# Optimization experiments

Hardware: AMD Instinct MI355X
Metric: run time of the kernel (lower is better)

Reference implementation:

```python
import jax, jax.numpy as jnp
import numpy as np

S, B, D, H, E, K, DF = 1024, 16, 512, 8, 16, 2, 2048
HD = D // H
EPS = 1e-5


def _layernorm(x, g, b):
    m = x.mean(-1, keepdims=True)
    v = ((x - m) ** 2).mean(-1, keepdims=True)
    return (x - m) / jnp.sqrt(v + EPS) * g + b


def setup_inputs() -> dict:
    key = jax.random.key(0)
    ks = jax.random.split(key, 10)
    s = 0.02
    return {
        "src": jax.random.normal(ks[0], (S, B, D), jnp.float32),
        "pos": jax.random.normal(ks[1], (S, B, D), jnp.float32),
        "in_proj_w": jax.random.normal(ks[2], (3 * D, D), jnp.float32) * s,
        "in_proj_b": jnp.zeros((3 * D,), jnp.float32),
        "out_w": jax.random.normal(ks[3], (D, D), jnp.float32) * s,
        "out_b": jnp.zeros((D,), jnp.float32),
        "norm1_g": jnp.ones((D,), jnp.float32),
        "norm1_b": jnp.zeros((D,), jnp.float32),
        "gate_w": jax.random.normal(ks[4], (E, D), jnp.float32) * s,
        "gate_b": jnp.zeros((E,), jnp.float32),
        "w1": jax.random.normal(ks[5], (E, DF, D), jnp.float32) * s,
        "b1": jnp.zeros((E, DF), jnp.float32),
        "w2": jax.random.normal(ks[6], (E, D, DF), jnp.float32) * s,
        "b2": jnp.zeros((E, D), jnp.float32),
    }


def reference(src, pos, in_proj_w, in_proj_b, out_w, out_b, norm1_g, norm1_b,
              gate_w, gate_b, w1, b1, w2, b2):
    # ---- self attention (torch nn.MultiheadAttention, seq-first) ----
    qk_in = src + pos                      # q = k = src + pos, v = src
    wq, wk, wv = jnp.split(in_proj_w, 3, axis=0)
    bq, bk, bv = jnp.split(in_proj_b, 3, axis=0)
    q = qk_in @ wq.T + bq                  # [S,B,D]
    k = qk_in @ wk.T + bk
    v = src @ wv.T + bv

    def heads(x):                          # [S,B,D] -> [B,H,S,HD]
        return x.reshape(S, B, H, HD).transpose(1, 2, 0, 3)

    qh, kh, vh = heads(q), heads(k), heads(v)
    scores = jnp.einsum('bhqd,bhkd->bhqk', qh * (1.0 / np.sqrt(HD)), kh)
    attn = jax.nn.softmax(scores, axis=-1)
    o = jnp.einsum('bhqk,bhkd->bhqd', attn, vh)
    o = o.transpose(2, 0, 1, 3).reshape(S, B, D) @ out_w.T + out_b

    x = _layernorm(src + o, norm1_g, norm1_b)  # post-norm residual

    # ---- MoE FFN (FMoE NaiveGate, top-k=2, no capacity drop) ----
    t = x.reshape(S * B, D)                # tokens
    logits = t @ gate_w.T + gate_b         # [T,E]
    topv, topi = jax.lax.top_k(logits, K)  # [T,K]
    gate_score = jax.nn.softmax(topv, axis=-1)
    T = S * B
    comb = jnp.zeros((T, E), t.dtype).at[jnp.arange(T)[:, None], topi].add(gate_score)

    def body(acc, packed):
        W1, B1, W2, B2, c = packed         # per-expert weights + combine col [T]
        h = jax.nn.relu(t @ W1.T + B1)     # [T,DF]
        y = h @ W2.T + B2                  # [T,D]
        return acc + c[:, None] * y, None

    acc, _ = jax.lax.scan(body, jnp.zeros_like(t), (w1, b1, w2, b2, comb.T))
    # pre_lnorm=False branch: output = inp + core_out (internal LN unused)
    return x + acc.reshape(S, B, D)
```

## Files before the change

kernel.cpp:

```cpp
#include <hip/hip_runtime.h>
#include <hip/hip_bf16.h>

typedef float f4 __attribute__((ext_vector_type(4)));
typedef float f32x4 __attribute__((ext_vector_type(4)));
typedef short short8 __attribute__((ext_vector_type(8)));
typedef unsigned short u16x4 __attribute__((ext_vector_type(4)));
typedef unsigned short u16x8 __attribute__((ext_vector_type(8)));
typedef unsigned int u32x4 __attribute__((ext_vector_type(4)));
typedef unsigned int u32x8 __attribute__((ext_vector_type(8)));

#define S_LEN 1024
#define BATCH 16
#define DIM   512
#define NH    8
#define HDIM  64
#define NE    16
#define DFF   2048
#define T_TOK 16384
#define CAP   34816
#define BM    128

__device__ __forceinline__ unsigned short f2bf(float f) {
  union { float f; unsigned u; } v; v.f = f;
  unsigned r = v.u + 0x7fffu + ((v.u >> 16) & 1u);
  return (unsigned short)(r >> 16);
}
__device__ __forceinline__ float bf2f(unsigned short h) {
  union { unsigned u; float f; } v; v.u = ((unsigned)h) << 16;
  return v.f;
}

__device__ __forceinline__ void load_lds16(const void* g, void* l) {
  __builtin_amdgcn_global_load_lds(
      (__attribute__((address_space(1))) void*)(void*)g,
      (__attribute__((address_space(3))) void*)l, 16, 0, 0);
}

__device__ __forceinline__ short8 pack_hi8(const unsigned* val) {
  union { unsigned u[4]; short8 s; } t;
#pragma unroll
  for (int i = 0; i < 4; i++)
    t.u[i] = (val[2 * i] >> 16) | (val[2 * i + 1] & 0xFFFF0000u);
  return t.s;
}
__device__ __forceinline__ short8 pack_lo8(const unsigned* val) {
  union { unsigned u[4]; short8 s; } t;
#pragma unroll
  for (int i = 0; i < 4; i++)
    t.u[i] = (val[2 * i] & 0xFFFFu) | (val[2 * i + 1] << 16);
  return t.s;
}

__global__ __launch_bounds__(256) void k_cvt_bf16(const float* __restrict__ in,
                                                  unsigned short* __restrict__ outb,
                                                  size_t n) {
  size_t i = ((size_t)blockIdx.x * 256 + threadIdx.x) * 4;
  size_t stride = (size_t)gridDim.x * 1024;
  for (; i < n; i += stride) {
    f4 v = *(const f4*)&in[i];
    u16x4 o;
    o[0] = f2bf(v[0]); o[1] = f2bf(v[1]); o[2] = f2bf(v[2]); o[3] = f2bf(v[3]);
    *(u16x4*)&outb[i] = o;
  }
}

__global__ __launch_bounds__(256) void k_split_w(const float* __restrict__ in,
                                                 unsigned short* __restrict__ hi,
                                                 unsigned short* __restrict__ lo,
                                                 size_t n) {
  size_t i = ((size_t)blockIdx.x * 256 + threadIdx.x) * 4;
  size_t stride = (size_t)gridDim.x * 1024;
  for (; i < n; i += stride) {
    f4 v = *(const f4*)&in[i];
    u16x4 h, l;
#pragma unroll
    for (int j = 0; j < 4; j++) {
      unsigned short hh = f2bf(v[j]);
      h[j] = hh;
      l[j] = f2bf(v[j] - bf2f(hh));
    }
    *(u16x4*)&hi[i] = h;
    *(u16x4*)&lo[i] = l;
  }
}

__global__ __launch_bounds__(64) void k_init(int* __restrict__ counts) {
  if (threadIdx.x < NE) counts[threadIdx.x] = 0;
}

__global__ __launch_bounds__(256) void k_zero_pad(const int* __restrict__ counts,
                                                  const int* __restrict__ off_pad,
                                                  unsigned short* __restrict__ Xg) {
  const int e = blockIdx.x;
  const int start = off_pad[e] + counts[e];
  const int end = off_pad[e + 1];
  for (int row = start; row < end; row++)
    *(unsigned int*)&Xg[(size_t)row * DIM + threadIdx.x * 2] = 0u;
}

__global__ __launch_bounds__(256, 2) void k_gemm_split(
    const float* __restrict__ A, const float* __restrict__ A2,
    const unsigned short* __restrict__ Wh, const unsigned short* __restrict__ Wl,
    const float* __restrict__ bias, int epi,
    unsigned* __restrict__ p0, unsigned* __restrict__ p1) {
  __shared__ __align__(16) char smem[33792];
  unsigned short* AhL = (unsigned short*)smem;
  unsigned short* AlL = (unsigned short*)(smem + 8192);
  unsigned short* WhL = (unsigned short*)(smem + 16384);
  unsigned short* WlL = (unsigned short*)(smem + 24576);
  unsigned* bounce = (unsigned*)smem;
  const int tid = threadIdx.x, lane = tid & 63, wid = tid >> 6;
  const int wm = wid >> 1, wn = wid & 1;
  const int m0 = blockIdx.x * 128, n0 = blockIdx.y * 128;
  const int row = tid >> 1, half = tid & 1;
  const int xr = (row >> 1) & 3;
  f32x4 acc[4][4] = {};
  f4 ar[4];
#pragma unroll
  for (int j = 0; j < 4; j++) {
    const size_t aoff = (size_t)(m0 + row) * 512 + half * 16 + j * 4;
    ar[j] = *(const f4*)&A[aoff];
    if (A2) { f4 v2 = *(const f4*)&A2[aoff]; ar[j] += v2; }
  }
  for (int k0 = 0; k0 < 512; k0 += 32) {
    __syncthreads();
    u16x8 hi8[2], lo8[2];
#pragma unroll
    for (int j = 0; j < 16; j++) {
      const float x = ar[j >> 2][j & 3];
      const unsigned short h = f2bf(x);
      hi8[j >> 3][j & 7] = h;
      lo8[j >> 3][j & 7] = f2bf(x - bf2f(h));
    }
    const int c0 = half * 2;
    *(u16x8*)&AhL[row * 32 + (((c0 + 0) ^ xr) << 3)] = hi8[0];
    *(u16x8*)&AhL[row * 32 + (((c0 + 1) ^ xr) << 3)] = hi8[1];
    *(u16x8*)&AlL[row * 32 + (((c0 + 0) ^ xr) << 3)] = lo8[0];
    *(u16x8*)&AlL[row * 32 + (((c0 + 1) ^ xr) << 3)] = lo8[1];
#pragma unroll
    for (int i = 0; i < 2; i++) {
      const int rowW = i * 64 + wid * 16 + (lane >> 2);
      const int clog = (lane & 3) ^ ((rowW >> 1) & 3);
      const size_t woff = (size_t)(n0 + rowW) * 512 + k0 + (clog << 3);
      load_lds16(Wh + woff, &WhL[i * 2048 + wid * 512]);
      load_lds16(Wl + woff, &WlL[i * 2048 + wid * 512]);
    }
    __syncthreads();
    if (k0 + 32 < 512) {
#pragma unroll
      for (int j = 0; j < 4; j++) {
        const size_t aoff = (size_t)(m0 + row) * 512 + k0 + 32 + half * 16 + j * 4;
        ar[j] = *(const f4*)&A[aoff];
        if (A2) { f4 v2 = *(const f4*)&A2[aoff]; ar[j] += v2; }
      }
    }
    const int l15 = lane & 15, lk = lane >> 4;
    const int xa = (l15 >> 1) & 3;
    short8 avh[4], avl[4], bvh[4], bvl[4];
#pragma unroll
    for (int mi = 0; mi < 4; mi++) {
      const int mr = wm * 64 + mi * 16 + l15;
      avh[mi] = *(const short8*)&AhL[mr * 32 + ((lk ^ xa) << 3)];
      avl[mi] = *(const short8*)&AlL[mr * 32 + ((lk ^ xa) << 3)];
    }
#pragma unroll
    for (int ni = 0; ni < 4; ni++) {
      const int nr = wn * 64 + ni * 16 + l15;
      bvh[ni] = *(const short8*)&WhL[nr * 32 + ((lk ^ xa) << 3)];
      bvl[ni] = *(const short8*)&WlL[nr * 32 + ((lk ^ xa) << 3)];
    }
#pragma unroll
    for (int mi = 0; mi < 4; mi++) {
#pragma unroll
      for (int ni = 0; ni < 4; ni++) {
        acc[mi][ni] = __builtin_amdgcn_mfma_f32_16x16x32_bf16(avh[mi], bvh[ni], acc[mi][ni], 0, 0, 0);
        acc[mi][ni] = __builtin_amdgcn_mfma_f32_16x16x32_bf16(avh[mi], bvl[ni], acc[mi][ni], 0, 0, 0);
        acc[mi][ni] = __builtin_amdgcn_mfma_f32_16x16x32_bf16(avl[mi], bvh[ni], acc[mi][ni], 0, 0, 0);
      }
    }
  }
  const int l15 = lane & 15, lq = lane >> 4;
  if (epi == 2) {
    float* of = (float*)p0;
#pragma unroll
    for (int mi = 0; mi < 4; mi++) {
      const int rb = m0 + wm * 64 + mi * 16 + (lq << 2);
#pragma unroll
      for (int ni = 0; ni < 4; ni++) {
        const int n = n0 + wn * 64 + ni * 16 + l15;
        const float bn = bias[n];
#pragma unroll
        for (int r = 0; r < 4; r++)
          of[(size_t)(rb + r) * 512 + n] = acc[mi][ni][r] + bn;
      }
    }
  } else if (epi == 0) {
#pragma unroll
    for (int mi = 0; mi < 4; mi++) {
      const int rb = m0 + wm * 64 + mi * 16 + (lq << 2);
#pragma unroll
      for (int ni = 0; ni < 4; ni++) {
        const int n = n0 + wn * 64 + ni * 16 + l15;
        const float bn = bias[n];
#pragma unroll
        for (int r = 0; r < 4; r++) {
          const int m = rb + r;
          const int bidx = m & 15, ss = m >> 4;
          float v = acc[mi][ni][r] + bn;
          unsigned* pl;
          int nn;
          if (n < 512) { v *= 0.125f; pl = p0; nn = n; }
          else { pl = p1; nn = n - 512; }
          const size_t off = ((size_t)(bidx * NH + (nn >> 6)) * S_LEN + ss) * HDIM + (nn & 63);
          const unsigned short hh = f2bf(v);
          pl[off] = ((unsigned)hh << 16) | (unsigned)f2bf(v - bf2f(hh));
        }
      }
    }
  } else {
    const int s_base = m0 >> 4;
    for (int halfn = 0; halfn < 2; halfn++) {
      __syncthreads();
      if (wn == halfn) {
#pragma unroll
        for (int mi = 0; mi < 4; mi++) {
          const int mlb = wm * 64 + mi * 16 + (lq << 2);
#pragma unroll
          for (int ni = 0; ni < 4; ni++) {
            const int n = n0 + wn * 64 + ni * 16 + l15;
            const float bn = bias[n];
            const int nc = ni * 16 + l15;
#pragma unroll
            for (int r = 0; r < 4; r++) {
              const float v = acc[mi][ni][r] + bn;
              const unsigned short hh = f2bf(v);
              bounce[(mlb + r) * 66 + nc] =
                  ((unsigned)hh << 16) | (unsigned)f2bf(v - bf2f(hh));
            }
          }
        }
      }
      __syncthreads();
#pragma unroll
      for (int i = 0; i < 4; i++) {
        const int idx = tid + 256 * i;
        const int nc = idx & 63, bb = idx >> 6;
        const int ng = n0 + halfn * 64 + nc;
        const int hh_ = ng >> 6, dd = ng & 63;
        u32x8 vals;
#pragma unroll
        for (int s = 0; s < 8; s++) vals[s] = bounce[(s * 16 + bb) * 66 + nc];
        *(u32x8*)&p0[((size_t)(bb * NH + hh_) * HDIM + dd) * S_LEN + s_base] = vals;
      }
    }
  }
}

__global__ __launch_bounds__(256, 4) void k_attn(
    const unsigned* __restrict__ Qp, const unsigned* __restrict__ Kp,
    const unsigned* __restrict__ Vp, float* __restrict__ O) {
  const int q0 = blockIdx.x * 64;
  const int bh = blockIdx.y;
  const int b = bh >> 3, h = bh & 7;
  const size_t base = (size_t)bh * (S_LEN * HDIM);
  __shared__ unsigned short KhL[64][72], KlL[64][72];
  __shared__ unsigned short VhL[64][72], VlL[64][72];
  const int tid = threadIdx.x, lane = tid & 63, w = tid >> 6;
  const int l15 = lane & 15, lq = lane >> 4;
  const int srcA = l15 + 16 * ((2 * lq) & 3);
  const int srcB = l15 + 16 * ((2 * lq + 1) & 3);
  const bool selHi = (lane & 32) != 0;
  short8 qh[2], ql[2];
  {
    const size_t qoff = base + (size_t)(q0 + 16 * w + l15) * HDIM + lq * 8;
    u32x8 qv0 = *(const u32x8*)&Qp[qoff];
    u32x8 qv1 = *(const u32x8*)&Qp[qoff + 32];
    qh[0] = pack_hi8((const unsigned*)&qv0); ql[0] = pack_lo8((const unsigned*)&qv0);
    qh[1] = pack_hi8((const unsigned*)&qv1); ql[1] = pack_lo8((const unsigned*)&qv1);
  }
  const int sr = tid >> 2, sq = (tid & 3) * 16;
  u32x4 kr[4], vr[4];
  {
    const size_t ko = base + (size_t)sr * HDIM + sq;
    const size_t vo = base + (size_t)sr * S_LEN + sq;
#pragma unroll
    for (int i = 0; i < 4; i++) {
      kr[i] = *(const u32x4*)&Kp[ko + 4 * i];
      vr[i] = *(const u32x4*)&Vp[vo + 4 * i];
    }
  }
  float m_ = -1e30f, l_ = 0.f;
  f32x4 acc[4] = {};

  for (int kt = 0; kt < 16; kt++) {
    {
      const unsigned* ku = (const unsigned*)kr;
      const unsigned* vu = (const unsigned*)vr;
      *(short8*)&KhL[sr][sq + 0] = pack_hi8(ku);
      *(short8*)&KhL[sr][sq + 8] = pack_hi8(ku + 8);
      *(short8*)&KlL[sr][sq + 0] = pack_lo8(ku);
      *(short8*)&KlL[sr][sq + 8] = pack_lo8(ku + 8);
      *(short8*)&VhL[sr][sq + 0] = pack_hi8(vu);
      *(short8*)&VhL[sr][sq + 8] = pack_hi8(vu + 8);
      *(short8*)&VlL[sr][sq + 0] = pack_lo8(vu);
      *(short8*)&VlL[sr][sq + 8] = pack_lo8(vu + 8);
    }
    __syncthreads();
    if (kt < 15) {
      const int s0n = (kt + 1) * 64;
      const size_t ko = base + (size_t)(s0n + sr) * HDIM + sq;
      const size_t vo = base + (size_t)sr * S_LEN + s0n + sq;
#pragma unroll
      for (int i = 0; i < 4; i++) {
        kr[i] = *(const u32x4*)&Kp[ko + 4 * i];
        vr[i] = *(const u32x4*)&Vp[vo + 4 * i];
      }
    }
    f32x4 sc[4] = {};
#pragma unroll
    for (int c = 0; c < 2; c++) {
      short8 kfh[4], kfl[4];
#pragma unroll
      for (int n = 0; n < 4; n++) {
        kfh[n] = *(const short8*)&KhL[16 * n + l15][c * 32 + lq * 8];
        kfl[n] = *(const short8*)&KlL[16 * n + l15][c * 32 + lq * 8];
      }
#pragma unroll
      for (int n = 0; n < 4; n++) {
        sc[n] = __builtin_amdgcn_mfma_f32_16x16x32_bf16(kfh[n], qh[c], sc[n], 0, 0, 0);
        sc[n] = __builtin_amdgcn_mfma_f32_16x16x32_bf16(kfl[n], qh[c], sc[n], 0, 0, 0);
        sc[n] = __builtin_amdgcn_mfma_f32_16x16x32_bf16(kfh[n], ql[c], sc[n], 0, 0, 0);
      }
    }
    float tm = fmaxf(fmaxf(fmaxf(sc[0][0], sc[0][1]), fmaxf(sc[0][2], sc[0][3])),
                     fmaxf(fmaxf(sc[1][0], sc[1][1]), fmaxf(sc[1][2], sc[1][3])));
    tm = fmaxf(tm, fmaxf(fmaxf(fmaxf(sc[2][0], sc[2][1]), fmaxf(sc[2][2], sc[2][3])),
                         fmaxf(fmaxf(sc[3][0], sc[3][1]), fmaxf(sc[3][2], sc[3][3]))));
    tm = fmaxf(tm, __shfl_xor(tm, 16));
    tm = fmaxf(tm, __shfl_xor(tm, 32));
    const float mn = fmaxf(m_, tm);
    const float esc = __expf(m_ - mn);
    m_ = mn;
    float rs = 0.f;
    unsigned pk[4][4];
#pragma unroll
    for (int n = 0; n < 4; n++) {
#pragma unroll
      for (int r = 0; r < 4; r++) {
        const float p = __expf(sc[n][r] - mn);
        rs += p;
        const unsigned short hh = f2bf(p);
        pk[n][r] = ((unsigned)hh << 16) | (unsigned)f2bf(p - bf2f(hh));
      }
    }
    rs += __shfl_xor(rs, 16);
    rs += __shfl_xor(rs, 32);
    l_ = l_ * esc + rs;
    float escR[4];
#pragma unroll
    for (int r = 0; r < 4; r++) escR[r] = __shfl(esc, 4 * lq + r);
#pragma unroll
    for (int n = 0; n < 4; n++) {
#pragma unroll
      for (int r = 0; r < 4; r++) acc[n][r] *= escR[r];
    }
#pragma unroll
    for (int c = 0; c < 2; c++) {
      unsigned val[8];
#pragma unroll
      for (int j = 0; j < 8; j++) {
        const int src = (j >> 2) ? srcB : srcA;
        const unsigned sA = (unsigned)__shfl((int)pk[2 * c + 0][j & 3], src);
        const unsigned sB = (unsigned)__shfl((int)pk[2 * c + 1][j & 3], src);
        val[j] = selHi ? sB : sA;
      }
      const short8 ph = pack_hi8(val);
      const short8 plo = pack_lo8(val);
      short8 vfh[4], vfl[4];
#pragma unroll
      for (int n = 0; n < 4; n++) {
        vfh[n] = *(const short8*)&VhL[16 * n + l15][c * 32 + lq * 8];
        vfl[n] = *(const short8*)&VlL[16 * n + l15][c * 32 + lq * 8];
      }
#pragma unroll
      for (int n = 0; n < 4; n++) {
        acc[n] = __builtin_amdgcn_mfma_f32_16x16x32_bf16(ph, vfh[n], acc[n], 0, 0, 0);
        acc[n] = __builtin_amdgcn_mfma_f32_16x16x32_bf16(ph, vfl[n], acc[n], 0, 0, 0);
        acc[n] = __builtin_amdgcn_mfma_f32_16x16x32_bf16(plo, vfh[n], acc[n], 0, 0, 0);
      }
    }
    __syncthreads();
  }
  const float inv = 1.f / l_;
  float invR[4];
#pragma unroll
  for (int r = 0; r < 4; r++) invR[r] = __shfl(inv, 4 * lq + r);
#pragma unroll
  for (int r = 0; r < 4; r++) {
    const int srow = q0 + 16 * w + 4 * lq + r;
    float* orow = &O[((size_t)srow * BATCH + b) * DIM + h * HDIM];
#pragma unroll
    for (int n = 0; n < 4; n++) orow[16 * n + l15] = acc[n][r] * invR[r];
  }
}

__global__ __launch_bounds__(256) void k_ln(const float* __restrict__ src,
                                            const float* __restrict__ proj,
                                            const float* __restrict__ g,
                                            const float* __restrict__ bt,
                                            float* __restrict__ xout) {
  const int wid = threadIdx.x >> 6, lane = threadIdx.x & 63;
  const int tok = blockIdx.x * 4 + wid;
  const size_t base = (size_t)tok * DIM + lane * 8;
  f4 a0 = *(const f4*)&src[base],  a1 = *(const f4*)&src[base + 4];
  f4 p0 = *(const f4*)&proj[base], p1 = *(const f4*)&proj[base + 4];
  float x[8];
  x[0] = a0[0] + p0[0]; x[1] = a0[1] + p0[1]; x[2] = a0[2] + p0[2]; x[3] = a0[3] + p0[3];
  x[4] = a1[0] + p1[0]; x[5] = a1[1] + p1[1]; x[6] = a1[2] + p1[2]; x[7] = a1[3] + p1[3];
  float s = 0.f, sq = 0.f;
#pragma unroll
  for (int j = 0; j < 8; j++) { s += x[j]; sq = fmaf(x[j], x[j], sq); }
#pragma unroll
  for (int d = 1; d < 64; d <<= 1) { s += __shfl_xor(s, d); sq += __shfl_xor(sq, d); }
  const float mean = s * (1.f / 512.f);
  const float var = sq * (1.f / 512.f) - mean * mean;
  const float rstd = 1.f / sqrtf(var + 1e-5f);
  const int ci = lane * 8;
  f4 o0v, o1v;
#pragma unroll
  for (int j = 0; j < 4; j++) o0v[j] = (x[j] - mean) * rstd * g[ci + j] + bt[ci + j];
#pragma unroll
  for (int j = 0; j < 4; j++) o1v[j] = (x[4 + j] - mean) * rstd * g[ci + 4 + j] + bt[ci + 4 + j];
  *(f4*)&xout[base] = o0v;
  *(f4*)&xout[base + 4] = o1v;
}

__global__ __launch_bounds__(256) void k_gate(const float* __restrict__ x,
                                              const float* __restrict__ gw,
                                              const float* __restrict__ gb,
                                              int* __restrict__ topi,
                                              float* __restrict__ topw,
                                              int* __restrict__ counts) {
  __shared__ float xs[16 * 520];
  __shared__ int hist[16];
  const int tid = threadIdx.x;
  const int tl = tid >> 4, e = tid & 15;
  if (tid < 16) hist[tid] = 0;
  const float gbe = gb[e];
  const float* wrow = gw + (size_t)e * DIM;
  for (int tile = 0; tile < 4; tile++) {
    const int t0 = blockIdx.x * 64 + tile * 16;
    __syncthreads();
    {
      const int r = tid >> 4, cbase = (tid & 15) * 32;
#pragma unroll
      for (int j = 0; j < 8; j++) {
        const int c = cbase + j * 4;
        const int ch = c >> 2;
        const int pc = ch ^ ((ch >> 3) & 7);
        *(f4*)&xs[r * 520 + pc * 4] = *(const f4*)&x[(size_t)(t0 + r) * DIM + c];
      }
    }
    __syncthreads();
    float d = gbe;
#pragma unroll 8
    for (int c = 0; c < DIM; c += 4) {
      const int ch = c >> 2;
      const int pc = ch ^ ((ch >> 3) & 7);
      f4 xv = *(const f4*)&xs[tl * 520 + pc * 4];
      f4 wv = *(const f4*)&wrow[c];
      d = fmaf(xv[0], wv[0], d); d = fmaf(xv[1], wv[1], d);
      d = fmaf(xv[2], wv[2], d); d = fmaf(xv[3], wv[3], d);
    }
    float v1 = d, v2 = -1e30f;
    int i1 = e, i2 = 1000;
#pragma unroll
    for (int s = 1; s < 16; s <<= 1) {
      const float ov1 = __shfl_xor(v1, s), ov2 = __shfl_xor(v2, s);
      const int oi1 = __shfl_xor(i1, s), oi2 = __shfl_xor(i2, s);
      if (ov1 > v1 || (ov1 == v1 && oi1 < i1)) {
        float nv2; int ni2;
        if (v1 > ov2 || (v1 == ov2 && i1 < oi2)) { nv2 = v1; ni2 = i1; }
        else { nv2 = ov2; ni2 = oi2; }
        v1 = ov1; i1 = oi1; v2 = nv2; i2 = ni2;
      } else if (ov1 > v2 || (ov1 == v2 && oi1 < i2)) {
        v2 = ov1; i2 = oi1;
      }
    }
    if (e == 0) {
      const int t = t0 + tl;
      const float e1 = __expf(v2 - v1);
      const float inv = 1.f / (1.f + e1);
      topi[2 * t] = i1;  topi[2 * t + 1] = i2;
      topw[2 * t] = inv; topw[2 * t + 1] = e1 * inv;
      atomicAdd(&hist[i1], 1);
      atomicAdd(&hist[i2], 1);
    }
  }
  __syncthreads();
  if (tid < 16 && hist[tid] > 0) atomicAdd(&counts[tid], hist[tid]);
}

__global__ void k_offsets(const int* __restrict__ counts,
                          int* __restrict__ off_pad, int* __restrict__ cursor) {
  if (threadIdx.x == 0) {
    int o = 0;
    off_pad[0] = 0;
    for (int e = 0; e < NE; e++) {
      cursor[e] = 0;
      o += ((counts[e] + BM - 1) / BM) * BM;
      off_pad[e + 1] = o;
    }
  }
}

__global__ __launch_bounds__(256) void k_scatter(const float* __restrict__ x,
                                                 const int* __restrict__ topi,
                                                 const int* __restrict__ off_pad,
                                                 int* __restrict__ cursor,
                                                 int* __restrict__ tokSlot,
                                                 unsigned short* __restrict__ Xg) {
  __shared__ int lcnt[16];
  __shared__ int gbase[16];
  __shared__ int posArr[128];
  const int tid = threadIdx.x;
  const int a0 = blockIdx.x * 128;
  if (tid < 16) lcnt[tid] = 0;
  __syncthreads();
  if (tid < 128) {
    const int a = a0 + tid;
    const int e = topi[a];
    const int lrank = atomicAdd(&lcnt[e], 1);
    posArr[tid] = (e << 24) | lrank;
  }
  __syncthreads();
  if (tid < 16) {
    const int c = lcnt[tid];
    gbase[tid] = (c > 0) ? atomicAdd(&cursor[tid], c) : 0;
  }
  __syncthreads();
  if (tid < 128) {
    const int a = a0 + tid;
    const int pk = posArr[tid];
    const int e = pk >> 24, lrank = pk & 0xffffff;
    const int pos = off_pad[e] + gbase[e] + lrank;
    posArr[tid] = pos;
    tokSlot[a] = pos;
  }
  __syncthreads();
  const int w = tid >> 6, lane = tid & 63;
#pragma unroll 4
  for (int i = 0; i < 32; i++) {
    const int idx = w * 32 + i;
    const int pos = posArr[idx];
    const int tok = (a0 + idx) >> 1;
    const size_t sb = (size_t)tok * DIM + lane * 8;
    f4 v0 = *(const f4*)&x[sb], v1 = *(const f4*)&x[sb + 4];
    u16x8 hh;
    hh[0] = f2bf(v0[0]); hh[1] = f2bf(v0[1]); hh[2] = f2bf(v0[2]); hh[3] = f2bf(v0[3]);
    hh[4] = f2bf(v1[0]); hh[5] = f2bf(v1[1]); hh[6] = f2bf(v1[2]); hh[7] = f2bf(v1[3]);
    *(u16x8*)&Xg[(size_t)pos * DIM + lane * 8] = hh;
  }
}

__global__ __launch_bounds__(256) void k_gemm_bf16(
    const unsigned short* __restrict__ A, int lda,
    const unsigned short* __restrict__ Wb, size_t westride, int ldw, int wrow0,
    const float* __restrict__ bias, int bstride, int brow0,
    int K, int epi,
    unsigned short* __restrict__ Hout, int ldh,
    const int* __restrict__ off_pad) {
  int bx = blockIdx.x;
  const int nwg = gridDim.x;
  if ((nwg & 7) == 0) bx = (bx & 7) * (nwg >> 3) + (bx >> 3);
  const int m0 = bx * BM;
  if (m0 >= off_pad[NE]) return;
  int e = 0;
  while (off_pad[e + 1] <= m0) e++;
  const unsigned short* W = Wb + (size_t)e * westride;
  const int n0 = blockIdx.y * 128;
  __shared__ unsigned short Al[128 * 64];
  __shared__ unsigned short Bl[128 * 64];
  const int tid = threadIdx.x, lane = tid & 63, wid = tid >> 6;
  const int wm = wid >> 1, wn = wid & 1;
  f32x4 acc[4][4] = {};
  const int srow = wid * 32 + (lane >> 3);
  const int scol = (((lane & 7) ^ ((lane >> 3) & 7)) << 3);
  for (int k0 = 0; k0 < K; k0 += 64) {
    const unsigned short* ga = A + (size_t)(m0 + srow) * lda + k0 + scol;
    const unsigned short* gw = W + (size_t)(wrow0 + n0 + srow) * ldw + k0 + scol;
#pragma unroll
    for (int i = 0; i < 4; i++) {
      load_lds16(ga + (size_t)i * 8 * lda, &Al[(wid * 32 + i * 8) * 64]);
      load_lds16(gw + (size_t)i * 8 * ldw, &Bl[(wid * 32 + i * 8) * 64]);
    }
    __syncthreads();
#pragma unroll
    for (int kk = 0; kk < 2; kk++) {
      short8 av[4], bv[4];
      const int ckx = (kk * 4 + (lane >> 4)) ^ (lane & 7);
#pragma unroll
      for (int mi = 0; mi < 4; mi++)
        av[mi] = *(const short8*)&Al[(wm * 64 + mi * 16 + (lane & 15)) * 64 + ckx * 8];
#pragma unroll
      for (int ni = 0; ni < 4; ni++)
        bv[ni] = *(const short8*)&Bl[(wn * 64 + ni * 16 + (lane & 15)) * 64 + ckx * 8];
#pragma unroll
      for (int mi = 0; mi < 4; mi++) {
#pragma unroll
        for (int ni = 0; ni < 4; ni++)
          acc[mi][ni] = __builtin_amdgcn_mfma_f32_16x16x32_bf16(av[mi], bv[ni], acc[mi][ni], 0, 0, 0);
      }
    }
    __syncthreads();
  }
#pragma unroll
  for (int mi = 0; mi < 4; mi++) {
    const int rb = m0 + wm * 64 + mi * 16 + ((lane >> 4) << 2);
#pragma unroll
    for (int ni = 0; ni < 4; ni++) {
      const int n = n0 + wn * 64 + ni * 16 + (lane & 15);
      const float bn = (epi != 2) ? bias[(size_t)e * bstride + brow0 + n] : 0.f;
      if (epi == 0) {
#pragma unroll
        for (int r = 0; r < 4; r++) {
          float v = acc[mi][ni][r] + bn;
          v = fmaxf(v, 0.f);
          Hout[(size_t)(rb + r) * ldh + n] = f2bf(v);
        }
      } else if (epi == 1) {
#pragma unroll
        for (int r = 0; r < 4; r++)
          Hout[(size_t)(rb + r) * ldh + n] = f2bf(acc[mi][ni][r] + bn);
      } else {
#pragma unroll
        for (int r = 0; r < 4; r++) {
          const size_t yo = (size_t)(rb + r) * ldh + n;
          Hout[yo] = f2bf(acc[mi][ni][r] + bf2f(Hout[yo]));
        }
      }
    }
  }
}

__global__ __launch_bounds__(256) void k_combine(const unsigned short* __restrict__ Y,
                                                 const int* __restrict__ tokSlot,
                                                 const float* __restrict__ topw,
                                                 float* __restrict__ out) {
  const int wid = threadIdx.x >> 6, lane = threadIdx.x & 63;
  const int t = blockIdx.x * 4 + wid;
  const int pa = tokSlot[2 * t], pb = tokSlot[2 * t + 1];
  const float wa = topw[2 * t], wb = topw[2 * t + 1];
  const size_t ob = (size_t)t * DIM + lane * 8;
  u16x8 ya = *(const u16x8*)&Y[(size_t)pa * DIM + lane * 8];
  u16x8 yb = *(const u16x8*)&Y[(size_t)pb * DIM + lane * 8];
  f4 o0 = *(const f4*)&out[ob], o1 = *(const f4*)&out[ob + 4];
#pragma unroll
  for (int j = 0; j < 4; j++) o0[j] += wa * bf2f(ya[j]) + wb * bf2f(yb[j]);
#pragma unroll
  for (int j = 0; j < 4; j++) o1[j] += wa * bf2f(ya[4 + j]) + wb * bf2f(yb[4 + j]);
  *(f4*)&out[ob] = o0;
  *(f4*)&out[ob + 4] = o1;
}

extern "C" void kernel_launch(void* const* d_in, const int* in_sizes, int n_in,
                              void* d_out, int out_size, void* d_ws, size_t ws_size,
                              hipStream_t stream) {
  const float* src       = (const float*)d_in[0];
  const float* pos       = (const float*)d_in[1];
  const float* in_proj_w = (const float*)d_in[2];
  const float* in_proj_b = (const float*)d_in[3];
  const float* out_w     = (const float*)d_in[4];
  const float* out_b     = (const float*)d_in[5];
  const float* norm1_g   = (const float*)d_in[6];
  const float* norm1_b   = (const float*)d_in[7];
  const float* gate_w    = (const float*)d_in[8];
  const float* gate_b    = (const float*)d_in[9];
  const float* w1        = (const float*)d_in[10];
  const float* b1        = (const float*)d_in[11];
  const float* w2        = (const float*)d_in[12];
  const float* b2        = (const float*)d_in[13];
  float* out = (float*)d_out;
  char* wsb = (char*)d_ws;

  unsigned* Qp = (unsigned*)(wsb + 0);
  unsigned* Kp = (unsigned*)(wsb + 33554432);
  unsigned* Vp = (unsigned*)(wsb + 67108864);
  float* ob = (float*)(wsb + 100663296);
  float* proj = (float*)(wsb + 0);
  unsigned short* w1b = (unsigned short*)(wsb + 0);
  unsigned short* w2b = (unsigned short*)(wsb + 33554432);
  unsigned short* Xg  = (unsigned short*)(wsb + 67108864);
  unsigned short* Hb  = (unsigned short*)(wsb + 102760448);
  unsigned short* Yb  = (unsigned short*)(wsb + 138412032);
  unsigned short* wih = (unsigned short*)(wsb + 134217728);
  unsigned short* wil = (unsigned short*)(wsb + 135790592);
  unsigned short* woh = (unsigned short*)(wsb + 137363456);
  unsigned short* wol = (unsigned short*)(wsb + 137887744);
  char* smallb = wsb + 174063616;
  int*   topi    = (int*)  (smallb + 0);
  float* topw    = (float*)(smallb + 131072);
  int*   tokSlot = (int*)  (smallb + 262144);
  int*   counts  = (int*)  (smallb + 540672);
  int*   off_pad = (int*)  (smallb + 540736);
  int*   cursor  = (int*)  (smallb + 540864);

  k_init<<<1, 64, 0, stream>>>(counts);
  k_split_w<<<768, 256, 0, stream>>>(in_proj_w, wih, wil, (size_t)1536 * 512);
  k_split_w<<<256, 256, 0, stream>>>(out_w, woh, wol, (size_t)512 * 512);
  k_gemm_split<<<dim3(128, 8), 256, 0, stream>>>(src, pos, wih, wil, in_proj_b, 0, Qp, Kp);
  k_gemm_split<<<dim3(128, 4), 256, 0, stream>>>(src, nullptr, wih + (size_t)1024 * 512,
                                                 wil + (size_t)1024 * 512, in_proj_b + 1024,
                                                 1, Vp, nullptr);
  k_attn<<<dim3(16, 128), 256, 0, stream>>>(Qp, Kp, Vp, ob);
  k_cvt_bf16<<<2048, 256, 0, stream>>>(w2, w2b, (size_t)NE * DIM * DFF);
  k_gemm_split<<<dim3(128, 4), 256, 0, stream>>>(ob, nullptr, woh, wol, out_b,
                                                 2, (unsigned*)proj, nullptr);
  k_ln<<<4096, 256, 0, stream>>>(src, proj, norm1_g, norm1_b, out);
  k_cvt_bf16<<<2048, 256, 0, stream>>>(w1, w1b, (size_t)NE * DFF * DIM);
  k_gate<<<T_TOK / 64, 256, 0, stream>>>(out, gate_w, gate_b, topi, topw, counts);
  k_offsets<<<1, 64, 0, stream>>>(counts, off_pad, cursor);
  k_zero_pad<<<NE, 256, 0, stream>>>(counts, off_pad, Xg);
  k_scatter<<<256, 256, 0, stream>>>(out, topi, off_pad, cursor, tokSlot, Xg);
  for (int p = 0; p < 4; ++p) {
    k_gemm_bf16<<<dim3(CAP / BM, 4), 256, 0, stream>>>(
        Xg, DIM, w1b, (size_t)DFF * DIM, DIM, p * 512,
        b1, DFF, p * 512, DIM, 0, Hb, 512, off_pad);
    k_gemm_bf16<<<dim3(CAP / BM, 4), 256, 0, stream>>>(
        Hb, 512, w2b + (size_t)p * 512, (size_t)DIM * DFF, DFF, 0,
        b2, DIM, 0, 512, (p == 0 ? 1 : 2), Yb, DIM, off_pad);
  }
  k_combine<<<T_TOK / 4, 256, 0, stream>>>(Yb, tokSlot, topw, out);
}
```

Measured before the change: 869.8 us.

## Pre-split activations into bf16 hi/lo and load A tiles directly to LDS

Adds a kernel that splits src+pos and src into bf16 hi/lo planes once, and has attention write its output as hi/lo bf16 planes. The split GEMM then stages A tiles with direct global-to-LDS loads, like the weights, instead of loading fp32 into registers and converting per tile. This moves the conversion work out of the GEMM inner loop, lowers register use (launch bounds raised to 3 blocks per CU), and shrinks the attention output. In exchange it adds an extra activation pass and more workspace traffic, and the register prefetch overlap of the next A tile is lost.

New measurement: 846.4 us (median of 2 runs). 2.7% less time.

```diff
diff --git a/kernel.cpp b/kernel.cpp
--- a/kernel.cpp
+++ b/kernel.cpp
@@ -84,6 +84,32 @@
   }
 }
 
+__global__ __launch_bounds__(256) void k_split_act(const float* __restrict__ src,
+                                                   const float* __restrict__ pos,
+                                                   unsigned short* __restrict__ Ah,
+                                                   unsigned short* __restrict__ Al,
+                                                   unsigned short* __restrict__ Sh,
+                                                   unsigned short* __restrict__ Sl) {
+  size_t i = ((size_t)blockIdx.x * 256 + threadIdx.x) * 4;
+  size_t stride = (size_t)gridDim.x * 1024;
+  const size_t n = (size_t)T_TOK * DIM;
+  for (; i < n; i += stride) {
+    f4 s = *(const f4*)&src[i];
+    f4 p = *(const f4*)&pos[i];
+    u16x4 ah, al, sh, sl;
+#pragma unroll
+    for (int j = 0; j < 4; j++) {
+      const float a = s[j] + p[j];
+      unsigned short hh = f2bf(a);
+      ah[j] = hh; al[j] = f2bf(a - bf2f(hh));
+      hh = f2bf(s[j]);
+      sh[j] = hh; sl[j] = f2bf(s[j] - bf2f(hh));
+    }
+    *(u16x4*)&Ah[i] = ah; *(u16x4*)&Al[i] = al;
+    *(u16x4*)&Sh[i] = sh; *(u16x4*)&Sl[i] = sl;
+  }
+}
+
 __global__ __launch_bounds__(64) void k_init(int* __restrict__ counts) {
   if (threadIdx.x < NE) counts[threadIdx.x] = 0;
 }
@@ -98,8 +124,8 @@
     *(unsigned int*)&Xg[(size_t)row * DIM + threadIdx.x * 2] = 0u;
 }
 
-__global__ __launch_bounds__(256, 2) void k_gemm_split(
-    const float* __restrict__ A, const float* __restrict__ A2,
+__global__ __launch_bounds__(256, 3) void k_gemm_split(
+    const unsigned short* __restrict__ Ah, const unsigned short* __restrict__ Al,
     const unsigned short* __restrict__ Wh, const unsigned short* __restrict__ Wl,
     const float* __restrict__ bias, int epi,
     unsigned* __restrict__ p0, unsigned* __restrict__ p1) {
@@ -112,48 +138,20 @@
   const int tid = threadIdx.x, lane = tid & 63, wid = tid >> 6;
   const int wm = wid >> 1, wn = wid & 1;
   const int m0 = blockIdx.x * 128, n0 = blockIdx.y * 128;
-  const int row = tid >> 1, half = tid & 1;
-  const int xr = (row >> 1) & 3;
   f32x4 acc[4][4] = {};
-  f4 ar[4];
-#pragma unroll
-  for (int j = 0; j < 4; j++) {
-    const size_t aoff = (size_t)(m0 + row) * 512 + half * 16 + j * 4;
-    ar[j] = *(const f4*)&A[aoff];
-    if (A2) { f4 v2 = *(const f4*)&A2[aoff]; ar[j] += v2; }
-  }
   for (int k0 = 0; k0 < 512; k0 += 32) {
-    __syncthreads();
-    u16x8 hi8[2], lo8[2];
-#pragma unroll
-    for (int j = 0; j < 16; j++) {
-      const float x = ar[j >> 2][j & 3];
-      const unsigned short h = f2bf(x);
-      hi8[j >> 3][j & 7] = h;
-      lo8[j >> 3][j & 7] = f2bf(x - bf2f(h));
-    }
-    const int c0 = half * 2;
-    *(u16x8*)&AhL[row * 32 + (((c0 + 0) ^ xr) << 3)] = hi8[0];
-    *(u16x8*)&AhL[row * 32 + (((c0 + 1) ^ xr) << 3)] = hi8[1];
-    *(u16x8*)&AlL[row * 32 + (((c0 + 0) ^ xr) << 3)] = lo8[0];
-    *(u16x8*)&AlL[row * 32 + (((c0 + 1) ^ xr) << 3)] = lo8[1];
 #pragma unroll
     for (int i = 0; i < 2; i++) {
-      const int rowW = i * 64 + wid * 16 + (lane >> 2);
-      const int clog = (lane & 3) ^ ((rowW >> 1) & 3);
-      const size_t woff = (size_t)(n0 + rowW) * 512 + k0 + (clog << 3);
+      const int rowT = i * 64 + wid * 16 + (lane >> 2);
+      const int clog = ((lane & 3) ^ ((rowT >> 1) & 3)) << 3;
+      const size_t aoff = (size_t)(m0 + rowT) * 512 + k0 + clog;
+      const size_t woff = (size_t)(n0 + rowT) * 512 + k0 + clog;
+      load_lds16(Ah + aoff, &AhL[i * 2048 + wid * 512]);
+      load_lds16(Al + aoff, &AlL[i * 2048 + wid * 512]);
       load_lds16(Wh + woff, &WhL[i * 2048 + wid * 512]);
       load_lds16(Wl + woff, &WlL[i * 2048 + wid * 512]);
     }
     __syncthreads();
-    if (k0 + 32 < 512) {
-#pragma unroll
-      for (int j = 0; j < 4; j++) {
-        const size_t aoff = (size_t)(m0 + row) * 512 + k0 + 32 + half * 16 + j * 4;
-        ar[j] = *(const f4*)&A[aoff];
-        if (A2) { f4 v2 = *(const f4*)&A2[aoff]; ar[j] += v2; }
-      }
-    }
     const int l15 = lane & 15, lk = lane >> 4;
     const int xa = (l15 >> 1) & 3;
     short8 avh[4], avl[4], bvh[4], bvl[4];
@@ -178,6 +176,7 @@
         acc[mi][ni] = __builtin_amdgcn_mfma_f32_16x16x32_bf16(avl[mi], bvh[ni], acc[mi][ni], 0, 0, 0);
       }
     }
+    __syncthreads();
   }
   const int l15 = lane & 15, lq = lane >> 4;
   if (epi == 2) {
@@ -258,7 +257,8 @@
 
 __global__ __launch_bounds__(256, 4) void k_attn(
     const unsigned* __restrict__ Qp, const unsigned* __restrict__ Kp,
-    const unsigned* __restrict__ Vp, float* __restrict__ O) {
+    const unsigned* __restrict__ Vp,
+    unsigned short* __restrict__ Oh, unsigned short* __restrict__ Ol) {
   const int q0 = blockIdx.x * 64;
   const int bh = blockIdx.y;
   const int b = bh >> 3, h = bh & 7;
@@ -398,9 +398,14 @@
 #pragma unroll
   for (int r = 0; r < 4; r++) {
     const int srow = q0 + 16 * w + 4 * lq + r;
-    float* orow = &O[((size_t)srow * BATCH + b) * DIM + h * HDIM];
-#pragma unroll
-    for (int n = 0; n < 4; n++) orow[16 * n + l15] = acc[n][r] * invR[r];
+    const size_t ro = ((size_t)srow * BATCH + b) * DIM + h * HDIM;
+#pragma unroll
+    for (int n = 0; n < 4; n++) {
+      const float v = acc[n][r] * invR[r];
+      const unsigned short hh = f2bf(v);
+      Oh[ro + 16 * n + l15] = hh;
+      Ol[ro + 16 * n + l15] = f2bf(v - bf2f(hh));
+    }
   }
 }
 
@@ -686,17 +691,22 @@
   unsigned* Qp = (unsigned*)(wsb + 0);
   unsigned* Kp = (unsigned*)(wsb + 33554432);
   unsigned* Vp = (unsigned*)(wsb + 67108864);
-  float* ob = (float*)(wsb + 100663296);
+  unsigned short* Ah = (unsigned short*)(wsb + 100663296);
+  unsigned short* Al = (unsigned short*)(wsb + 117440512);
+  unsigned short* Oh = (unsigned short*)(wsb + 100663296);
+  unsigned short* Ol = (unsigned short*)(wsb + 117440512);
+  unsigned short* Sh = (unsigned short*)(wsb + 134217728);
+  unsigned short* Sl = (unsigned short*)(wsb + 150994944);
+  unsigned short* wih = (unsigned short*)(wsb + 167772160);
+  unsigned short* wil = (unsigned short*)(wsb + 169345024);
+  unsigned short* woh = (unsigned short*)(wsb + 170917888);
+  unsigned short* wol = (unsigned short*)(wsb + 171442176);
   float* proj = (float*)(wsb + 0);
   unsigned short* w1b = (unsigned short*)(wsb + 0);
   unsigned short* w2b = (unsigned short*)(wsb + 33554432);
   unsigned short* Xg  = (unsigned short*)(wsb + 67108864);
   unsigned short* Hb  = (unsigned short*)(wsb + 102760448);
   unsigned short* Yb  = (unsigned short*)(wsb + 138412032);
-  unsigned short* wih = (unsigned short*)(wsb + 134217728);
-  unsigned short* wil = (unsigned short*)(wsb + 135790592);
-  unsigned short* woh = (unsigned short*)(wsb + 137363456);
-  unsigned short* wol = (unsigned short*)(wsb + 137887744);
   char* smallb = wsb + 174063616;
   int*   topi    = (int*)  (smallb + 0);
   float* topw    = (float*)(smallb + 131072);
@@ -708,13 +718,14 @@
   k_init<<<1, 64, 0, stream>>>(counts);
   k_split_w<<<768, 256, 0, stream>>>(in_proj_w, wih, wil, (size_t)1536 * 512);
   k_split_w<<<256, 256, 0, stream>>>(out_w, woh, wol, (size_t)512 * 512);
-  k_gemm_split<<<dim3(128, 8), 256, 0, stream>>>(src, pos, wih, wil, in_proj_b, 0, Qp, Kp);
-  k_gemm_split<<<dim3(128, 4), 256, 0, stream>>>(src, nullptr, wih + (size_t)1024 * 512,
+  k_split_act<<<2048, 256, 0, stream>>>(src, pos, Ah, Al, Sh, Sl);
+  k_gemm_split<<<dim3(128, 8), 256, 0, stream>>>(Ah, Al, wih, wil, in_proj_b, 0, Qp, Kp);
+  k_gemm_split<<<dim3(128, 4), 256, 0, stream>>>(Sh, Sl, wih + (size_t)1024 * 512,
                                                  wil + (size_t)1024 * 512, in_proj_b + 1024,
                                                  1, Vp, nullptr);
-  k_attn<<<dim3(16, 128), 256, 0, stream>>>(Qp, Kp, Vp, ob);
+  k_attn<<<dim3(16, 128), 256, 0, stream>>>(Qp, Kp, Vp, Oh, Ol);
   k_cvt_bf16<<<2048, 256, 0, stream>>>(w2, w2b, (size_t)NE * DIM * DFF);
-  k_gemm_split<<<dim3(128, 4), 256, 0, stream>>>(ob, nullptr, woh, wol, out_b,
+  k_gemm_split<<<dim3(128, 4), 256, 0, stream>>>(Oh, Ol, woh, wol, out_b,
                                                  2, (unsigned*)proj, nullptr);
   k_ln<<<4096, 256, 0, stream>>>(src, proj, norm1_g, norm1_b, out);
   k_cvt_bf16<<<2048, 256, 0, stream>>>(w1, w1b, (size_t)NE * DFF * DIM);
```
